# Optimization experiments

Measured on AMD Instinct MI355X. Metric: run time of the kernel, lower is better.

## Reference

```python
import jax, jax.numpy as jnp
import numpy as np

B, S, D, H, HD, R = 1, 3072, 2048, 16, 128, 16
ALPHA = 16.0
EPS = 1e-6


def _rope_freqs():
    # standard RoPE angles, interleave-duplicated so freqs[..., 0::2] gives the
    # per-pair cos values exactly as the torch module slices them
    inv = 1.0 / (10000.0 ** (np.arange(0, HD, 2, dtype=np.float32) / HD))  # [HD/2]
    ang = np.arange(S, dtype=np.float32)[:, None] * inv[None, :]           # [S, HD/2]
    cos = np.repeat(np.cos(ang), 2, axis=-1).reshape(1, S, 1, HD)
    sin = np.repeat(np.sin(ang), 2, axis=-1).reshape(1, S, 1, HD)
    return jnp.asarray(cos), jnp.asarray(sin)


def setup_inputs() -> dict:
    key = jax.random.key(0)
    ks = jax.random.split(key, 18)
    n = jax.random.normal
    WS = 0.02  # weight init scale
    freqs_cos, freqs_sin = _rope_freqs()
    return {
        "hidden_states": n(ks[0], (B, S, D), jnp.float32),
        "wq": n(ks[1], (D, D), jnp.float32) * WS,
        "bq": n(ks[2], (D,), jnp.float32) * WS,
        "wk": n(ks[3], (D, D), jnp.float32) * WS,
        "bk": n(ks[4], (D,), jnp.float32) * WS,
        "wv": n(ks[5], (D, D), jnp.float32) * WS,
        "bv": n(ks[6], (D,), jnp.float32) * WS,
        "wo": n(ks[7], (D, D), jnp.float32) * WS,
        "bo": n(ks[8], (D,), jnp.float32) * WS,
        "lq_down": n(ks[9], (R, D), jnp.float32) / R,
        "lq_up": n(ks[10], (D, R), jnp.float32) * WS,
        "lk_down": n(ks[11], (R, D), jnp.float32) / R,
        "lk_up": n(ks[12], (D, R), jnp.float32) * WS,
        "lv_down": n(ks[13], (R, D), jnp.float32) / R,
        "lv_up": n(ks[14], (D, R), jnp.float32) * WS,
        "lo_down": n(ks[15], (R, D), jnp.float32) / R,
        "lo_up": n(ks[16], (D, R), jnp.float32) * WS,
        "norm_q_w": jnp.ones((D,), jnp.float32),
        "norm_k_w": jnp.ones((D,), jnp.float32),
        "freqs_cos": freqs_cos,
        "freqs_sin": freqs_sin,
    }


def _lora(x, w_down, w_up, scale):
    return (x @ w_down.T) @ w_up.T * scale


def _rmsnorm(x, w):
    return x * jax.lax.rsqrt(jnp.mean(x * x, axis=-1, keepdims=True) + EPS) * w


def _apply_rotary(x, freqs_cos, freqs_sin):
    # x: [B,S,H,HD]; freqs: [1,S,1,HD]
    x1, x2 = x[..., 0::2], x[..., 1::2]
    c = freqs_cos[..., 0::2]
    s = freqs_sin[..., 1::2]
    even = x1 * c - x2 * s
    odd = x1 * s + x2 * c
    return jnp.stack([even, odd], axis=-1).reshape(x.shape)


def reference(hidden_states, wq, bq, wk, bk, wv, bv, wo, bo,
              lq_down, lq_up, lk_down, lk_up, lv_down, lv_up, lo_down, lo_up,
              norm_q_w, norm_k_w, freqs_cos, freqs_sin):
    scale = ALPHA / R
    x = hidden_states
    # qkv projections + LoRA adds (self-attention: encoder_hidden_states = hidden_states)
    q = x @ wq.T + bq + _lora(x, lq_down, lq_up, scale)
    k = x @ wk.T + bk + _lora(x, lk_down, lk_up, scale)
    v = x @ wv.T + bv + _lora(x, lv_down, lv_up, scale)
    # RMSNorm over full d_model, then split heads
    q = _rmsnorm(q, norm_q_w).reshape(B, S, H, HD)
    k = _rmsnorm(k, norm_k_w).reshape(B, S, H, HD)
    v = v.reshape(B, S, H, HD)
    # custom strided rotary embedding
    q = _apply_rotary(q, freqs_cos, freqs_sin)
    k = _apply_rotary(k, freqs_cos, freqs_sin)
    # SDPA (non-causal, no mask)
    scores = jnp.einsum('bihd,bjhd->bhij', q, k) / jnp.sqrt(jnp.float32(HD))
    attn = jax.nn.softmax(scores, axis=-1)
    o = jnp.einsum('bhij,bjhd->bihd', attn, v).reshape(B, S, D)
    # output projection + LoRA
    out = o @ wo.T + bo + _lora(o, lo_down, lo_up, scale)
    return out
```

## Files before the change

kernel.cpp:

```cpp
#include <hip/hip_runtime.h>
#include <stdint.h>

#define S_LEN 3072
#define DIM   2048
#define NH    16
#define HDIM  128
#define RANK  16
#define EPS_F 1e-6f
#define LORA_SCALE 1.0f
#define QK_SCALE 0.08838834764831845f
#define SM_MAX 24.0f
#define L2E 1.4426950408889634f

typedef unsigned short u16;
typedef __attribute__((ext_vector_type(8))) short short8;
typedef __attribute__((ext_vector_type(4))) float f32x4;
typedef __attribute__((ext_vector_type(16))) float f32x16;
typedef __attribute__((ext_vector_type(4))) unsigned short u16x4;
typedef __attribute__((ext_vector_type(8))) unsigned short u16x8;
typedef __attribute__((ext_vector_type(2))) unsigned short u16x2;
typedef __attribute__((ext_vector_type(4))) float float4a;
typedef __attribute__((ext_vector_type(4))) unsigned int uint4a;

__device__ __forceinline__ u16 f2b(float f) {
  uint32_t u = __builtin_bit_cast(uint32_t, f);
  u += 0x7fffu + ((u >> 16) & 1u);
  return (u16)(u >> 16);
}
__device__ __forceinline__ float b2f(u16 b) {
  uint32_t u = ((uint32_t)b) << 16;
  return __builtin_bit_cast(float, u);
}

__device__ __forceinline__ unsigned cvt_pk_bf16(float lo, float hi) {
  unsigned r;
  asm("v_cvt_pk_bf16_f32 %0, %1, %2" : "=v"(r) : "v"(lo), "v"(hi));
  return r;
}
__device__ __forceinline__ void pl32_swap(unsigned& a, unsigned& b) {
  asm("v_permlane32_swap_b32 %0, %1" : "+v"(a), "+v"(b));
}

__device__ __forceinline__ void g2l16(const void* g, void* l) {
  __builtin_amdgcn_global_load_lds(
      (__attribute__((address_space(1))) unsigned int*)g,
      (__attribute__((address_space(3))) unsigned int*)l, 16, 0, 0);
}

__global__ __launch_bounds__(256) void convf2b(const float* __restrict__ in,
                                               u16* __restrict__ out) {
  int i = (blockIdx.x * 256 + threadIdx.x) * 4;
  float4a v = *(const float4a*)(in + i);
  u16x4 o = { f2b(v[0]), f2b(v[1]), f2b(v[2]), f2b(v[3]) };
  *(u16x4*)(out + i) = o;
}

__global__ __launch_bounds__(256) void fold_lora4(
    const float* __restrict__ w0, const float* __restrict__ w1,
    const float* __restrict__ w2, const float* __restrict__ w3,
    const float* __restrict__ u0, const float* __restrict__ u1,
    const float* __restrict__ u2, const float* __restrict__ u3,
    const float* __restrict__ d0, const float* __restrict__ d1,
    const float* __restrict__ d2, const float* __restrict__ d3,
    u16* __restrict__ out_qkv, u16* __restrict__ out_o) {
  const int z = blockIdx.z;
  const float* W  = (z == 0) ? w0 : (z == 1) ? w1 : (z == 2) ? w2 : w3;
  const float* lu = (z == 0) ? u0 : (z == 1) ? u1 : (z == 2) ? u2 : u3;
  const float* ld = (z == 0) ? d0 : (z == 1) ? d1 : (z == 2) ? d2 : d3;
  u16* out = (z < 3) ? out_qkv + (size_t)z * DIM * DIM : out_o;
  __shared__ float lds_ld[16][136];
  __shared__ float lds_lu[64][17];
  const int tid = threadIdx.x;
  const int k0 = blockIdx.x * 128, n0 = blockIdx.y * 64;
  {
    int idx = tid * 8, r = idx >> 7, c = idx & 127;
    const float* src = ld + r * DIM + k0 + c;
#pragma unroll
    for (int e = 0; e < 8; ++e) lds_ld[r][c + e] = src[e];
  }
  {
    int idx = tid * 4, n = idx >> 4, r4 = idx & 15;
    const float* src = lu + (size_t)(n0 + n) * RANK + r4;
#pragma unroll
    for (int e = 0; e < 4; ++e) lds_lu[n][r4 + e] = src[e];
  }
  __syncthreads();
  const int n = tid >> 2;
  const int kg = (tid & 3) * 32;
  float luv[RANK];
#pragma unroll
  for (int r = 0; r < RANK; ++r) luv[r] = lds_lu[n][r];
  const float* wrow = W + (size_t)(n0 + n) * DIM + k0 + kg;
  u16* orow = out + (size_t)(n0 + n) * DIM + k0 + kg;
#pragma unroll
  for (int j = 0; j < 8; ++j) {
    float4a acc = *(const float4a*)(wrow + j * 4);
#pragma unroll
    for (int r = 0; r < RANK; ++r) {
      float4a lv = *(const float4a*)&lds_ld[r][kg + j * 4];
      acc += LORA_SCALE * luv[r] * lv;
    }
    u16x4 o = { f2b(acc[0]), f2b(acc[1]), f2b(acc[2]), f2b(acc[3]) };
    *(u16x4*)(orow + j * 4) = o;
  }
}

__global__ __launch_bounds__(256, 4) void gemm_fused(
    const u16* __restrict__ A, const u16* __restrict__ B,
    const float* __restrict__ b0, const float* __restrict__ b1,
    const float* __restrict__ b2, u16* __restrict__ c0, u16* __restrict__ c1,
    u16* __restrict__ c2t, float* __restrict__ Cf) {
  __shared__ __attribute__((aligned(16))) u16 As[128 * 64];
  __shared__ __attribute__((aligned(16))) u16 Bs[128 * 64];
  const int tid = threadIdx.x;
  const int wave = tid >> 6, lane = tid & 63;
  const int quad = lane >> 4, l15 = lane & 15;
  int nwg = gridDim.x * gridDim.y;
  int flat = blockIdx.y * gridDim.x + blockIdx.x;
  int cpx = nwg >> 3;
  int swz = (flat & 7) * cpx + (flat >> 3);
  const int m0 = (swz % gridDim.x) * 128;
  const int n0 = (swz / gridDim.x) * 128;
  const int mat = n0 >> 11;
  const float* bias = (mat == 0) ? b0 : (mat == 1 ? b1 : b2);
  u16* Cb = (mat == 0) ? c0 : c1;
  const int wr = wave >> 1, wc = wave & 1;
  f32x4 acc[4][4] = {};
  for (int kt = 0; kt < DIM / 64; ++kt) {
    __syncthreads();
#pragma unroll
    for (int i = 0; i < 4; ++i) {
      int chunk = i * 256 + wave * 64 + lane;
      int row = chunk >> 3, c8 = chunk & 7;
      int cg = c8 ^ (row & 7);
      g2l16(A + (size_t)(m0 + row) * DIM + kt * 64 + cg * 8,
            As + (i * 256 + wave * 64) * 8);
      g2l16(B + (size_t)(n0 + row) * DIM + kt * 64 + cg * 8,
            Bs + (i * 256 + wave * 64) * 8);
    }
    __syncthreads();
#pragma unroll
    for (int kc = 0; kc < 2; ++kc) {
      short8 af[4], bf[4];
#pragma unroll
      for (int tm = 0; tm < 4; ++tm)
        af[tm] = *(const short8*)(As + (wr * 64 + tm * 16 + l15) * 64 +
                                  (((kc * 2 + (quad >> 1)) * 2 + (quad & 1)) ^
                                   (l15 & 7)) * 8);
#pragma unroll
      for (int tn = 0; tn < 4; ++tn)
        bf[tn] = *(const short8*)(Bs + (wc * 64 + tn * 16 + l15) * 64 +
                                  (((kc * 2 + (quad >> 1)) * 2 + (quad & 1)) ^
                                   (l15 & 7)) * 8);
#pragma unroll
      for (int tm = 0; tm < 4; ++tm)
#pragma unroll
        for (int tn = 0; tn < 4; ++tn)
          acc[tm][tn] = __builtin_amdgcn_mfma_f32_16x16x32_bf16(
              af[tm], bf[tn], acc[tm][tn], 0, 0, 0);
    }
  }
#pragma unroll
  for (int tn = 0; tn < 4; ++tn) {
    int col = n0 + wc * 64 + tn * 16 + l15;
    int colL = col & (DIM - 1);
    float bcol = bias[colL];
#pragma unroll
    for (int tm = 0; tm < 4; ++tm) {
      int row0 = m0 + wr * 64 + tm * 16 + quad * 4;
      if (Cf) {
#pragma unroll
        for (int r = 0; r < 4; ++r)
          Cf[(size_t)(row0 + r) * DIM + colL] = acc[tm][tn][r] + bcol;
      } else if (mat == 2) {
        u16x4 o = { f2b(acc[tm][tn][0] + bcol), f2b(acc[tm][tn][1] + bcol),
                    f2b(acc[tm][tn][2] + bcol), f2b(acc[tm][tn][3] + bcol) };
        *(u16x4*)(c2t + (size_t)colL * S_LEN + row0) = o;
      } else {
#pragma unroll
        for (int r = 0; r < 4; ++r)
          Cb[(size_t)(row0 + r) * DIM + colL] = f2b(acc[tm][tn][r] + bcol);
      }
    }
  }
}

__global__ __launch_bounds__(256) void rms_rope(
    u16* __restrict__ q, u16* __restrict__ k,
    const float* __restrict__ nqw, const float* __restrict__ nkw,
    const float* __restrict__ fc, const float* __restrict__ fs) {
  const int s = blockIdx.x, tid = threadIdx.x;
  const int wave = tid >> 6, lane = tid & 63;
  float qv[8], kv[8];
  float sq = 0.f, sk = 0.f;
#pragma unroll
  for (int i = 0; i < 4; ++i) {
    int p = i * 256 + tid;
    u16x2 qa = *(const u16x2*)(q + (size_t)s * DIM + 2 * p);
    u16x2 ka = *(const u16x2*)(k + (size_t)s * DIM + 2 * p);
    qv[2 * i] = b2f(qa[0]); qv[2 * i + 1] = b2f(qa[1]);
    kv[2 * i] = b2f(ka[0]); kv[2 * i + 1] = b2f(ka[1]);
    sq += qv[2 * i] * qv[2 * i] + qv[2 * i + 1] * qv[2 * i + 1];
    sk += kv[2 * i] * kv[2 * i] + kv[2 * i + 1] * kv[2 * i + 1];
  }
#pragma unroll
  for (int off = 32; off > 0; off >>= 1) {
    sq += __shfl_down(sq, off);
    sk += __shfl_down(sk, off);
  }
  __shared__ float part[2][4];
  if (lane == 0) { part[0][wave] = sq; part[1][wave] = sk; }
  __syncthreads();
  float sumq = part[0][0] + part[0][1] + part[0][2] + part[0][3];
  float sumk = part[1][0] + part[1][1] + part[1][2] + part[1][3];
  float rq = rsqrtf(sumq * (1.f / DIM) + EPS_F);
  float rk = rsqrtf(sumk * (1.f / DIM) + EPS_F);
#pragma unroll
  for (int i = 0; i < 4; ++i) {
    int p = i * 256 + tid;
    int ip = p & 63;
    float c = fc[s * HDIM + 2 * ip];
    float sn = fs[s * HDIM + 2 * ip + 1];
    float e = qv[2 * i] * rq * nqw[2 * p];
    float o = qv[2 * i + 1] * rq * nqw[2 * p + 1];
    u16x2 qo = { f2b((e * c - o * sn) * QK_SCALE),
                 f2b((e * sn + o * c) * QK_SCALE) };
    *(u16x2*)(q + (size_t)s * DIM + 2 * p) = qo;
    float e2 = kv[2 * i] * rk * nkw[2 * p];
    float o2 = kv[2 * i + 1] * rk * nkw[2 * p + 1];
    u16x2 ko = { f2b(e2 * c - o2 * sn), f2b(e2 * sn + o2 * c) };
    *(u16x2*)(k + (size_t)s * DIM + 2 * p) = ko;
  }
}

__global__ __launch_bounds__(256, 2) void flash_attn(
    const u16* __restrict__ qb, const u16* __restrict__ kb,
    const u16* __restrict__ vt, u16* __restrict__ ob) {
  __shared__ __attribute__((aligned(16))) u16 Ks[64 * 128];
  __shared__ __attribute__((aligned(16))) u16 Vt[128 * 64];
  const int tid = threadIdx.x;
  const int wave = tid >> 6, lane = tid & 63;
  const int l31 = lane & 31, hi = lane >> 5;
  const int q0 = blockIdx.x * 128, h = blockIdx.y;
  short8 qf[8];
  {
    const u16* qrow =
        qb + (size_t)(q0 + wave * 32 + l31) * DIM + h * HDIM + hi * 8;
#pragma unroll
    for (int kc = 0; kc < 8; ++kc) qf[kc] = *(const short8*)(qrow + kc * 16);
  }
  f32x16 of[4] = {};
  float sP = 0.f;
  for (int it = 0; it < S_LEN / 64; ++it) {
    const int j0 = it * 64;
    __syncthreads();
#pragma unroll
    for (int i = 0; i < 4; ++i) {
      int slot = i * 256 + tid;
      {
        int j = slot >> 4, csp = slot & 15;
        int cg = csp ^ (j & 7);
        g2l16(kb + (size_t)(j0 + j) * DIM + h * HDIM + cg * 8,
              Ks + (i * 256 + wave * 64) * 8);
      }
      {
        int d = slot >> 3, cbp = slot & 7;
        int cbg = cbp ^ (d & 7);
        g2l16(vt + (size_t)(h * HDIM + d) * S_LEN + j0 + cbg * 8,
              Vt + (i * 256 + wave * 64) * 8);
      }
    }
    __syncthreads();
    f32x16 sf[2] = {};
    __builtin_amdgcn_s_setprio(1);
#pragma unroll
    for (int kc = 0; kc < 8; ++kc) {
      int gc = kc * 2 + hi;
#pragma unroll
      for (int mt = 0; mt < 2; ++mt) {
        int j = mt * 32 + l31;
        short8 kf = *(const short8*)(Ks + j * 128 + (gc ^ (j & 7)) * 8);
        sf[mt] =
            __builtin_amdgcn_mfma_f32_32x32x16_bf16(kf, qf[kc], sf[mt], 0, 0, 0);
      }
    }
    __builtin_amdgcn_s_setprio(0);
    short8 pb[4];
#pragma unroll
    for (int mt = 0; mt < 2; ++mt) {
      float p[16];
#pragma unroll
      for (int r = 0; r < 16; ++r)
        p[r] = exp2f(fmaf(sf[mt][r], L2E, -SM_MAX * L2E));
      float t0 = (p[0] + p[1]) + (p[2] + p[3]);
      float t1 = (p[4] + p[5]) + (p[6] + p[7]);
      float t2 = (p[8] + p[9]) + (p[10] + p[11]);
      float t3 = (p[12] + p[13]) + (p[14] + p[15]);
      sP += (t0 + t1) + (t2 + t3);
      unsigned w[8];
#pragma unroll
      for (int g = 0; g < 8; ++g) w[g] = cvt_pk_bf16(p[2 * g], p[2 * g + 1]);
      pl32_swap(w[0], w[2]);
      pl32_swap(w[1], w[3]);
      pl32_swap(w[4], w[6]);
      pl32_swap(w[5], w[7]);
      uint4a fe = { w[0], w[1], w[2], w[3] };
      uint4a fo = { w[4], w[5], w[6], w[7] };
      pb[2 * mt] = __builtin_bit_cast(short8, fe);
      pb[2 * mt + 1] = __builtin_bit_cast(short8, fo);
    }
    __builtin_amdgcn_s_setprio(1);
#pragma unroll
    for (int kc = 0; kc < 4; ++kc) {
      int gj = kc * 2 + hi;
#pragma unroll
      for (int mt2 = 0; mt2 < 4; ++mt2) {
        int d = mt2 * 32 + l31;
        short8 vf = *(const short8*)(Vt + d * 64 + (gj ^ (d & 7)) * 8);
        of[mt2] =
            __builtin_amdgcn_mfma_f32_32x32x16_bf16(vf, pb[kc], of[mt2], 0, 0, 0);
      }
    }
    __builtin_amdgcn_s_setprio(0);
  }
  float inv = 1.f / (sP + __shfl_xor(sP, 32));
  const int q = q0 + wave * 32 + l31;
#pragma unroll
  for (int mt2 = 0; mt2 < 4; ++mt2) {
#pragma unroll
    for (int t = 0; t < 4; ++t) {
      u16x4 o = { f2b(of[mt2][4 * t + 0] * inv), f2b(of[mt2][4 * t + 1] * inv),
                  f2b(of[mt2][4 * t + 2] * inv), f2b(of[mt2][4 * t + 3] * inv) };
      *(u16x4*)(ob + (size_t)q * DIM + h * HDIM + mt2 * 32 + t * 8 + hi * 4) = o;
    }
  }
}

extern "C" void kernel_launch(void* const* d_in, const int* in_sizes, int n_in,
                              void* d_out, int out_size, void* d_ws,
                              size_t ws_size, hipStream_t stream) {
  (void)in_sizes; (void)n_in; (void)out_size; (void)ws_size;
  const float* x   = (const float*)d_in[0];
  const float* wq  = (const float*)d_in[1];
  const float* bq  = (const float*)d_in[2];
  const float* wk  = (const float*)d_in[3];
  const float* bk  = (const float*)d_in[4];
  const float* wv  = (const float*)d_in[5];
  const float* bv  = (const float*)d_in[6];
  const float* wo  = (const float*)d_in[7];
  const float* bo  = (const float*)d_in[8];
  const float* lqd = (const float*)d_in[9];
  const float* lqu = (const float*)d_in[10];
  const float* lkd = (const float*)d_in[11];
  const float* lku = (const float*)d_in[12];
  const float* lvd = (const float*)d_in[13];
  const float* lvu = (const float*)d_in[14];
  const float* lod = (const float*)d_in[15];
  const float* lou = (const float*)d_in[16];
  const float* nqw = (const float*)d_in[17];
  const float* nkw = (const float*)d_in[18];
  const float* fc  = (const float*)d_in[19];
  const float* fs  = (const float*)d_in[20];

  char* ws = (char*)d_ws;
  size_t off = 0;
  auto alloc = [&](size_t bytes) {
    void* p = ws + off;
    off += (bytes + 255) & ~(size_t)255;
    return p;
  };
  const size_t SD2 = (size_t)S_LEN * DIM * 2;
  const size_t WW  = (size_t)DIM * DIM;
  u16* xb    = (u16*)alloc(SD2);
  u16* wqkvb = (u16*)alloc(3 * WW * 2);
  u16* wob   = (u16*)alloc(WW * 2);
  u16* q16   = (u16*)alloc(SD2);
  u16* k16   = (u16*)alloc(SD2);
  u16* vbT   = (u16*)alloc(SD2);
  u16* ob    = (u16*)alloc(SD2);

  convf2b<<<S_LEN * DIM / 1024, 256, 0, stream>>>(x, xb);
  fold_lora4<<<dim3(DIM / 128, DIM / 64, 4), 256, 0, stream>>>(
      wq, wk, wv, wo, lqu, lku, lvu, lou, lqd, lkd, lvd, lod, wqkvb, wob);
  gemm_fused<<<dim3(S_LEN / 128, 3 * DIM / 128), 256, 0, stream>>>(
      xb, wqkvb, bq, bk, bv, q16, k16, vbT, nullptr);
  rms_rope<<<S_LEN, 256, 0, stream>>>(q16, k16, nqw, nkw, fc, fs);
  flash_attn<<<dim3(S_LEN / 128, NH), 256, 0, stream>>>(q16, k16, vbT, ob);
  gemm_fused<<<dim3(S_LEN / 128, DIM / 128), 256, 0, stream>>>(
      ob, wob, bo, nullptr, nullptr, nullptr, nullptr, nullptr, (float*)d_out);
}
```

Measured before the change: 451.5 us.

## Split flash attention over KV into two partitions with a combine kernel

Adds a KV-split dimension to the attention grid so each block processes half the keys. Each block writes unnormalized fp32 partial outputs and row sums, and a new combine kernel sums them, normalizes, and converts to bf16. This is meant to raise the block count and fill more CUs. The cost is extra fp32 memory traffic and an additional kernel launch.

```diff
diff --git a/kernel.cpp b/kernel.cpp
--- a/kernel.cpp
+++ b/kernel.cpp
@@ -11,6 +11,7 @@
 #define QK_SCALE 0.08838834764831845f
 #define SM_MAX 24.0f
 #define L2E 1.4426950408889634f
+#define KVSPLIT 2
 
 typedef unsigned short u16;
 typedef __attribute__((ext_vector_type(8))) short short8;
@@ -235,13 +236,17 @@
 
 __global__ __launch_bounds__(256, 2) void flash_attn(
     const u16* __restrict__ qb, const u16* __restrict__ kb,
-    const u16* __restrict__ vt, u16* __restrict__ ob) {
+    const u16* __restrict__ vt, float* __restrict__ opart,
+    float* __restrict__ spart) {
   __shared__ __attribute__((aligned(16))) u16 Ks[64 * 128];
   __shared__ __attribute__((aligned(16))) u16 Vt[128 * 64];
   const int tid = threadIdx.x;
   const int wave = tid >> 6, lane = tid & 63;
   const int l31 = lane & 31, hi = lane >> 5;
-  const int q0 = blockIdx.x * 128, h = blockIdx.y;
+  const int q0 = blockIdx.x * 128, h = blockIdx.y, kvh = blockIdx.z;
+  float* op = opart + (size_t)kvh * S_LEN * DIM;
+  float* sp = spart + (size_t)kvh * S_LEN * NH;
+  const int NT = S_LEN / (64 * KVSPLIT);
   short8 qf[8];
   {
     const u16* qrow =
@@ -251,8 +256,8 @@
   }
   f32x16 of[4] = {};
   float sP = 0.f;
-  for (int it = 0; it < S_LEN / 64; ++it) {
-    const int j0 = it * 64;
+  for (int it = 0; it < NT; ++it) {
+    const int j0 = (kvh * NT + it) * 64;
     __syncthreads();
 #pragma unroll
     for (int i = 0; i < 4; ++i) {
@@ -323,17 +328,35 @@
     }
     __builtin_amdgcn_s_setprio(0);
   }
-  float inv = 1.f / (sP + __shfl_xor(sP, 32));
   const int q = q0 + wave * 32 + l31;
+  float s = sP + __shfl_xor(sP, 32);
+  if (lane < 32) sp[(size_t)q * NH + h] = s;
 #pragma unroll
   for (int mt2 = 0; mt2 < 4; ++mt2) {
 #pragma unroll
     for (int t = 0; t < 4; ++t) {
-      u16x4 o = { f2b(of[mt2][4 * t + 0] * inv), f2b(of[mt2][4 * t + 1] * inv),
-                  f2b(of[mt2][4 * t + 2] * inv), f2b(of[mt2][4 * t + 3] * inv) };
-      *(u16x4*)(ob + (size_t)q * DIM + h * HDIM + mt2 * 32 + t * 8 + hi * 4) = o;
-    }
-  }
+      float4a o = { of[mt2][4 * t + 0], of[mt2][4 * t + 1],
+                    of[mt2][4 * t + 2], of[mt2][4 * t + 3] };
+      *(float4a*)(op + (size_t)q * DIM + h * HDIM + mt2 * 32 + t * 8 +
+                  hi * 4) = o;
+    }
+  }
+}
+
+__global__ __launch_bounds__(256) void comb(const float* __restrict__ o0,
+                                            const float* __restrict__ o1,
+                                            const float* __restrict__ s0,
+                                            const float* __restrict__ s1,
+                                            u16* __restrict__ ob) {
+  size_t i = ((size_t)blockIdx.x * 256 + threadIdx.x) * 4;
+  int q = (int)(i >> 11);
+  int h = (int)((i >> 7) & (NH - 1));
+  float inv = 1.f / (s0[(size_t)q * NH + h] + s1[(size_t)q * NH + h]);
+  float4a a = *(const float4a*)(o0 + i);
+  float4a b = *(const float4a*)(o1 + i);
+  u16x4 o = { f2b((a[0] + b[0]) * inv), f2b((a[1] + b[1]) * inv),
+              f2b((a[2] + b[2]) * inv), f2b((a[3] + b[3]) * inv) };
+  *(u16x4*)(ob + i) = o;
 }
 
 extern "C" void kernel_launch(void* const* d_in, const int* in_sizes, int n_in,
@@ -370,6 +393,7 @@
     return p;
   };
   const size_t SD2 = (size_t)S_LEN * DIM * 2;
+  const size_t SD4 = (size_t)S_LEN * DIM * 4;
   const size_t WW  = (size_t)DIM * DIM;
   u16* xb    = (u16*)alloc(SD2);
   u16* wqkvb = (u16*)alloc(3 * WW * 2);
@@ -378,6 +402,8 @@
   u16* k16   = (u16*)alloc(SD2);
   u16* vbT   = (u16*)alloc(SD2);
   u16* ob    = (u16*)alloc(SD2);
+  float* opart = (float*)alloc(KVSPLIT * SD4);
+  float* spart = (float*)alloc(KVSPLIT * S_LEN * NH * 4);
 
   convf2b<<<S_LEN * DIM / 1024, 256, 0, stream>>>(x, xb);
   fold_lora4<<<dim3(DIM / 128, DIM / 64, 4), 256, 0, stream>>>(
@@ -385,7 +411,11 @@
   gemm_fused<<<dim3(S_LEN / 128, 3 * DIM / 128), 256, 0, stream>>>(
       xb, wqkvb, bq, bk, bv, q16, k16, vbT, nullptr);
   rms_rope<<<S_LEN, 256, 0, stream>>>(q16, k16, nqw, nkw, fc, fs);
-  flash_attn<<<dim3(S_LEN / 128, NH), 256, 0, stream>>>(q16, k16, vbT, ob);
+  flash_attn<<<dim3(S_LEN / 128, NH, KVSPLIT), 256, 0, stream>>>(
+      q16, k16, vbT, opart, spart);
+  comb<<<S_LEN * DIM / 1024, 256, 0, stream>>>(
+      opart, opart + (size_t)S_LEN * DIM, spart, spart + (size_t)S_LEN * NH,
+      ob);
   gemm_fused<<<dim3(S_LEN / 128, DIM / 128), 256, 0, stream>>>(
       ob, wob, bo, nullptr, nullptr, nullptr, nullptr, nullptr, (float*)d_out);
 }
```

Result: slower. 480.1 us (+6.4%).
